# Kernel optimization log

Measured on AMD Instinct MI355X. Metric: run time of the kernel, lower is better.

The kernel has to match this reference:

```python
import jax, jax.numpy as jnp
import numpy as np
import math

EMBED = 256
NH = 8            # num_heads
HD = EMBED // NH  # head_dim = 32
LEVELS = 4
P = 4             # points per level
SUMP = LEVELS * P # 16
OFFSET_SCALE = 0.5
SPATIAL = ((80, 80), (40, 40), (20, 20), (10, 10))  # (H, W) per level
BS, LQ = 4, 4096
LV = sum(h * w for h, w in SPATIAL)  # 8500


def _offset_bias():
    # replicates _reset_parameters grid init for sampling_offsets.bias
    thetas = np.arange(NH, dtype=np.float32) * (2.0 * math.pi / NH)
    grid = np.stack([np.cos(thetas), np.sin(thetas)], -1)  # [NH,2]
    grid = grid / np.abs(grid).max(-1, keepdims=True)
    grid = np.tile(grid.reshape(NH, 1, 2), (1, SUMP, 1))   # [NH,SUMP,2]
    scaling = np.concatenate([np.arange(1, P + 1) for _ in range(LEVELS)]).reshape(1, SUMP, 1)
    grid = grid * scaling
    return jnp.asarray(grid.reshape(-1), dtype=jnp.float32)  # [NH*SUMP*2]


def setup_inputs() -> dict:
    key = jax.random.key(0)
    ks = jax.random.split(key, 8)
    xavier = lambda k, fi, fo: jax.random.uniform(k, (fi, fo), jnp.float32,
                                                  -math.sqrt(6.0 / (fi + fo)), math.sqrt(6.0 / (fi + fo)))
    return {
        "query": jax.random.normal(ks[0], (BS, LQ, EMBED), jnp.float32),
        "reference_points": jax.random.uniform(ks[1], (BS, LQ, 1, 4), jnp.float32),
        "value": jax.random.normal(ks[2], (BS, LV, EMBED), jnp.float32),
        # sampling_offsets: weight is zero-init in torch; use small random so offsets depend on query
        "W_off": jax.random.normal(ks[3], (EMBED, NH * SUMP * 2), jnp.float32) * 0.01,
        "b_off": _offset_bias(),
        "W_attn": jax.random.normal(ks[4], (EMBED, NH * SUMP), jnp.float32) * 0.01,
        "b_attn": jnp.zeros((NH * SUMP,), jnp.float32),
        "W_v": xavier(ks[5], EMBED, EMBED),
        "b_v": jnp.zeros((EMBED,), jnp.float32),
        "W_o": xavier(ks[6], EMBED, EMBED),
        "b_o": jnp.zeros((EMBED,), jnp.float32),
    }


def _bilinear_sample(v_l, loc, Hl, Wl):
    """grid_sample (bilinear, zero padding, align_corners=False) on one level.
    v_l: [bs, NH, Hl*Wl, HD]; loc: [bs, Lq, NH, P, 2] in [0,1] (x=width, y=height).
    Returns [bs, Lq, NH, P, HD]."""
    bs, lq, nh, p, _ = loc.shape
    x = loc[..., 0] * Wl - 0.5
    y = loc[..., 1] * Hl - 0.5
    x0 = jnp.floor(x)
    y0 = jnp.floor(y)
    lx, ly = x - x0, y - y0
    x0i = x0.astype(jnp.int32)
    y0i = y0.astype(jnp.int32)

    def corner(xi, yi, w):
        valid = ((xi >= 0) & (xi < Wl) & (yi >= 0) & (yi < Hl)).astype(v_l.dtype)
        idx = jnp.clip(yi, 0, Hl - 1) * Wl + jnp.clip(xi, 0, Wl - 1)  # [bs,Lq,NH,P]
        idx = jnp.transpose(idx, (0, 2, 1, 3)).reshape(bs, nh, lq * p)
        g = jnp.take_along_axis(v_l, idx[..., None], axis=2)          # [bs,NH,Lq*P,HD]
        g = g.reshape(bs, nh, lq, p, HD).transpose(0, 2, 1, 3, 4)     # [bs,Lq,NH,P,HD]
        return g * (w * valid)[..., None]

    return (corner(x0i, y0i, (1 - lx) * (1 - ly))
            + corner(x0i + 1, y0i, lx * (1 - ly))
            + corner(x0i, y0i + 1, (1 - lx) * ly)
            + corner(x0i + 1, y0i + 1, lx * ly))


def reference(query, reference_points, value, W_off, b_off, W_attn, b_attn, W_v, b_v, W_o, b_o):
    bs, lq = query.shape[:2]
    lv = value.shape[1]

    v = (value @ W_v + b_v).reshape(bs, lv, NH, HD)

    off = (query @ W_off + b_off).reshape(bs, lq, NH, SUMP, 2)
    attn = jax.nn.softmax((query @ W_attn + b_attn).reshape(bs, lq, NH, SUMP), axis=-1)

    # reference_points last dim == 4 path (box refs)
    nps = jnp.full((SUMP, 1), 1.0 / P, dtype=query.dtype)  # num_points_scale
    loc = (reference_points[:, :, None, :, :2]
           + off * nps * reference_points[:, :, None, :, 2:] * OFFSET_SCALE)  # [bs,Lq,NH,SUMP,2]

    out = jnp.zeros((bs, lq, NH, HD), dtype=query.dtype)
    v_start, p_start = 0, 0
    for (Hl, Wl) in SPATIAL:
        n = Hl * Wl
        v_l = jnp.transpose(v[:, v_start:v_start + n], (0, 2, 1, 3))  # [bs,NH,n,HD]
        loc_l = loc[:, :, :, p_start:p_start + P]
        w_l = attn[:, :, :, p_start:p_start + P]
        sampled = _bilinear_sample(v_l, loc_l, Hl, Wl)                # [bs,Lq,NH,P,HD]
        out = out + jnp.einsum('blhpd,blhp->blhd', sampled, w_l)
        v_start += n
        p_start += P

    return out.reshape(bs, lq, EMBED) @ W_o + b_o
```

## Files before the change

kernel.cpp:

```cpp
#include <hip/hip_runtime.h>

#define NH 8
#define HD 32
#define SUMP 16
#define LQ 4096
#define BS 4
#define LV 8500
#define NQ (BS * LQ)
#define MV (BS * LV)

typedef float f32x4 __attribute__((ext_vector_type(4)));
typedef _Float16 f16x8 __attribute__((ext_vector_type(8)));

__global__ __launch_bounds__(256) void prep_kernel(
    const float* __restrict__ Wv, const float* __restrict__ Woff,
    const float* __restrict__ Wattn, const float* __restrict__ Wo,
    const float* __restrict__ boff, const float* __restrict__ battn,
    _Float16* __restrict__ WtVf, _Float16* __restrict__ WtOAf,
    _Float16* __restrict__ WtOf, float* __restrict__ biasOA)
{
    int g = blockIdx.x * 256 + threadIdx.x;
    int gl; _Float16* dst; int which;
    if (g < 65536)       { gl = g;          dst = WtVf;  which = 0; }
    else if (g < 163840) { gl = g - 65536;  dst = WtOAf; which = 1; }
    else                 { gl = g - 163840; dst = WtOf;  which = 2; }
    int e = gl & 7, m16 = (gl >> 3) & 15, q = (gl >> 7) & 3, C = (gl >> 9) & 7, T = gl >> 12;
    int n = T * 16 + m16, k = C * 32 + q * 8 + e;
    float w;
    if (which == 0)      w = Wv[k * 256 + n];
    else if (which == 1) w = (n < 256) ? Woff[k * 256 + n] : Wattn[k * 128 + (n - 256)];
    else                 w = Wo[k * 256 + n];
    dst[gl] = (_Float16)w;
    if (blockIdx.x == 0) biasOA[threadIdx.x] = boff[threadIdx.x];
    if (blockIdx.x == 1 && threadIdx.x < 128) biasOA[256 + threadIdx.x] = battn[threadIdx.x];
}

__device__ __forceinline__ f16x8 cvt8(const float4& lo, const float4& hi) {
    f16x8 r;
    r[0] = (_Float16)lo.x; r[1] = (_Float16)lo.y; r[2] = (_Float16)lo.z; r[3] = (_Float16)lo.w;
    r[4] = (_Float16)hi.x; r[5] = (_Float16)hi.y; r[6] = (_Float16)hi.z; r[7] = (_Float16)hi.w;
    return r;
}

template <int NI, bool V_MODE, bool A_F16>
__device__ __forceinline__ void chunk_gemm(
    const float* __restrict__ A32, const _Float16* __restrict__ A16,
    const _Float16* __restrict__ Bf, const float* __restrict__ bias,
    void* __restrict__ Cv, int M, int N, int mchunk, int ntbase,
    _Float16* __restrict__ As )
{
    const int t = threadIdx.x;
    const int wave = t >> 6, lane = t & 63;
    const int quad = lane >> 4, l16 = lane & 15;

    {
        const int srow = t >> 2, schunk = t & 3;
        int gr = mchunk * 64 + srow;
        if (gr > M - 1) gr = M - 1;
        if (A_F16) {
            const _Float16* src = A16 + (size_t)gr * 256 + schunk * 64;
            f16x8 hb[8];
            #pragma unroll
            for (int j = 0; j < 8; ++j) hb[j] = *(const f16x8*)(src + j * 8);
            #pragma unroll
            for (int j = 0; j < 8; ++j) {
                int slot = (schunk * 8 + j) ^ (srow & 7);
                *(f16x8*)(As + srow * 256 + slot * 8) = hb[j];
            }
        } else {
            const float* src = A32 + (size_t)gr * 256 + schunk * 64;
            float4 buf[16];
            #pragma unroll
            for (int j = 0; j < 16; ++j) buf[j] = *(const float4*)(src + j * 4);
            #pragma unroll
            for (int j = 0; j < 8; ++j) {
                f16x8 h = cvt8(buf[2 * j], buf[2 * j + 1]);
                int slot = (schunk * 8 + j) ^ (srow & 7);
                *(f16x8*)(As + srow * 256 + slot * 8) = h;
            }
        }
    }
    __syncthreads();

    const int ntile0 = ntbase + wave * NI;
    const _Float16* bp[NI];
    #pragma unroll
    for (int ni = 0; ni < NI; ++ni)
        bp[ni] = Bf + (size_t)(ntile0 + ni) * 4096 + lane * 8;

    f16x8 bcur[NI], bnxt[NI];
    f32x4 acc[4][NI] = {};
    #pragma unroll
    for (int ni = 0; ni < NI; ++ni) bcur[ni] = *(const f16x8*)(bp[ni]);

    #pragma unroll
    for (int k = 0; k < 8; ++k) {
        if (k < 7) {
            #pragma unroll
            for (int ni = 0; ni < NI; ++ni) bnxt[ni] = *(const f16x8*)(bp[ni] + (k + 1) * 512);
        }
        f16x8 af[4];
        #pragma unroll
        for (int mi = 0; mi < 4; ++mi) {
            int row = mi * 16 + l16;
            int slot = (quad + k * 4) ^ (row & 7);
            af[mi] = *(const f16x8*)(As + row * 256 + slot * 8);
        }
        #pragma unroll
        for (int mi = 0; mi < 4; ++mi)
            #pragma unroll
            for (int ni = 0; ni < NI; ++ni)
                acc[mi][ni] = __builtin_amdgcn_mfma_f32_16x16x32_f16(af[mi], bcur[ni], acc[mi][ni], 0, 0, 0);
        if (k < 7) {
            #pragma unroll
            for (int ni = 0; ni < NI; ++ni) bcur[ni] = bnxt[ni];
        }
    }

    if (V_MODE) {
        #pragma unroll
        for (int mi = 0; mi < 4; ++mi) {
            int mq = mchunk * 64 + mi * 16 + quad * 4;
            size_t rb[4]; int vld[4];
            #pragma unroll
            for (int r = 0; r < 4; ++r) {
                int m = mq + r;
                vld[r] = (m < M);
                int mm = vld[r] ? m : 0;
                int b = mm / LV; int pos = mm - b * LV;
                rb[r] = ((size_t)b * NH * LV + pos) * 32;
            }
            #pragma unroll
            for (int ni = 0; ni < NI; ++ni) {
                int n = (ntile0 + ni) * 16 + l16;
                float bv = bias[n];
                int h = n >> 5, d = n & 31;
                size_t ho = (size_t)h * (LV * 32) + d;
                #pragma unroll
                for (int r = 0; r < 4; ++r)
                    if (vld[r]) ((_Float16*)Cv)[rb[r] + ho] = (_Float16)(acc[mi][ni][r] + bv);
            }
        }
    } else {
        #pragma unroll
        for (int ni = 0; ni < NI; ++ni) {
            int n = (ntile0 + ni) * 16 + l16;
            float bv = bias[n];
            #pragma unroll
            for (int mi = 0; mi < 4; ++mi) {
                int mq = mchunk * 64 + mi * 16 + quad * 4;
                #pragma unroll
                for (int r = 0; r < 4; ++r)
                    ((float*)Cv)[(size_t)(mq + r) * N + n] = acc[mi][ni][r] + bv;
            }
        }
    }
}

__global__ __launch_bounds__(256) void gemm_dual_kernel(
    const float* __restrict__ value, const _Float16* __restrict__ WtVf,
    const float* __restrict__ b_v, _Float16* __restrict__ v_f16,
    const float* __restrict__ query, const _Float16* __restrict__ WtOAf,
    const float* __restrict__ biasOA, float* __restrict__ oa)
{
    __shared__ __align__(16) _Float16 As[64 * 256];
    int bid = blockIdx.x;
    if (bid < 532) {
        chunk_gemm<4, true, false>(value, nullptr, WtVf, b_v, v_f16, MV, 256,
                                   bid, 0, As);
    } else {
        int g = bid - 532;
        chunk_gemm<3, false, false>(query, nullptr, WtOAf, biasOA, oa, NQ, 384,
                                    g >> 1, (g & 1) * 12, As);
    }
}

__global__ __launch_bounds__(256) void gemm_o_kernel(
    const _Float16* __restrict__ mid, const _Float16* __restrict__ WtOf,
    const float* __restrict__ b_o, float* __restrict__ out)
{
    __shared__ __align__(16) _Float16 As[64 * 256];
    chunk_gemm<4, false, true>(nullptr, mid, WtOf, b_o, out, NQ, 256,
                               blockIdx.x, 0, As);
}

__global__ void sample_kernel(
    const _Float16* __restrict__ v,
    const float* __restrict__ oa,
    const float* __restrict__ refp,
    _Float16* __restrict__ mid)
{
    const int blk = blockIdx.x;
    const int xcd = blk & 7, j = blk >> 3;
    const int bh = xcd * 4 + (j & 3);
    const int chunk = j >> 2;
    const int b = bh >> 3, h = bh & 7;
    const int rowG0 = b * LQ + chunk * 16;

    const int t = threadIdx.x;
    const int wave = t >> 6, lane = t & 63;

    __shared__ __align__(16) int2   s_pk[16 * 17];
    __shared__ __align__(16) float4 s_w4[16 * 17];
    __shared__ __align__(16) float  s_part[2 * 8 * 32];

    {
        int task = t >> 4, p = t & 15, l = p >> 2;
        int row = rowG0 + task;
        float4 r4 = *(const float4*)(refp + (size_t)row * 4);
        float2 o2 = *(const float2*)(oa + (size_t)row * 384 + (h * 16 + p) * 2);
        float raw = oa[(size_t)row * 384 + 256 + h * 16 + p];

        float mx = raw;
        #pragma unroll
        for (int d = 8; d >= 1; d >>= 1) mx = fmaxf(mx, __shfl_xor(mx, d, 16));
        float ex = __expf(raw - mx);
        float sm = ex;
        #pragma unroll
        for (int d = 8; d >= 1; d >>= 1) sm += __shfl_xor(sm, d, 16);
        float w = ex * __builtin_amdgcn_rcpf(sm);

        int Wl = 80 >> l;
        int vst = (l == 0) ? 0 : (l == 1) ? 6400 : (l == 2) ? 8000 : 8400;
        float x = (r4.x + o2.x * 0.125f * r4.z) * Wl - 0.5f;
        float y = (r4.y + o2.y * 0.125f * r4.w) * Wl - 0.5f;
        float x0f = floorf(x), y0f = floorf(y);
        float lx = x - x0f, ly = y - y0f;
        int x0 = (int)x0f, y0 = (int)y0f;
        int x1 = x0 + 1, y1 = y0 + 1;
        float mx0 = (x0 >= 0 && x0 < Wl) ? 1.f : 0.f;
        float mx1 = (x1 >= 0 && x1 < Wl) ? 1.f : 0.f;
        float my0 = (y0 >= 0 && y0 < Wl) ? 1.f : 0.f;
        float my1 = (y1 >= 0 && y1 < Wl) ? 1.f : 0.f;
        int cx0 = min(max(x0, 0), Wl - 1), cx1 = min(max(x1, 0), Wl - 1);
        int cy0 = min(max(y0, 0), Wl - 1), cy1 = min(max(y1, 0), Wl - 1);
        int2 r_pk;
        float4 r_w4;
        r_pk.x = (vst + cy0 * Wl + cx0) * 64;
        r_pk.y = ((cx1 - cx0) * 64) | (((cy1 - cy0) * Wl * 64) << 16);
        r_w4.x = w * (1.f - lx) * (1.f - ly) * mx0 * my0;
        r_w4.y = w * lx * (1.f - ly) * mx1 * my0;
        r_w4.z = w * (1.f - lx) * ly * mx0 * my1;
        r_w4.w = w * lx * ly * mx1 * my1;
        int s = task * 17 + p;
        s_pk[s] = r_pk; s_w4[s] = r_w4;
    }
    __syncthreads();

    {
        const int wg = wave >> 1, wp = wave & 1;
        const int pgl = lane >> 5, tk = (lane >> 2) & 7, dv2 = lane & 3;
        const int task = wg * 8 + tk;
        const int row = rowG0 + task;
        const char* vb = (const char*)v + ((size_t)(b * NH + h) * LV) * 64 + dv2 * 16;

        int2 pk[4]; float4 w4[4];
        #pragma unroll
        for (int jj = 0; jj < 4; ++jj) {
            int p = (wp * 2 + pgl) * 4 + jj;
            int s = task * 17 + p;
            pk[jj] = s_pk[s]; w4[jj] = s_w4[s];
        }
        f16x8 g0[4], g1[4], g2[4], g3[4];
        #pragma unroll
        for (int jj = 0; jj < 4; ++jj) {
            int dx = pk[jj].y & 0xffff, dy = pk[jj].y >> 16;
            const char* base = vb + pk[jj].x;
            g0[jj] = *(const f16x8*)(base);
            g1[jj] = *(const f16x8*)(base + dx);
            g2[jj] = *(const f16x8*)(base + dy);
            g3[jj] = *(const f16x8*)(base + dx + dy);
        }
        float acc8[8] = {};
        #pragma unroll
        for (int jj = 0; jj < 4; ++jj)
            #pragma unroll
            for (int c = 0; c < 8; ++c)
                acc8[c] += w4[jj].x * (float)g0[jj][c] + w4[jj].y * (float)g1[jj][c]
                         + w4[jj].z * (float)g2[jj][c] + w4[jj].w * (float)g3[jj][c];

        #pragma unroll
        for (int c = 0; c < 8; ++c) acc8[c] += __shfl_xor(acc8[c], 32, 64);
        if (wp == 1 && lane < 32) {
            #pragma unroll
            for (int c = 0; c < 8; ++c) s_part[wg * 256 + c * 32 + lane] = acc8[c];
        }
        __syncthreads();
        if (wp == 0 && lane < 32) {
            f16x8 m8;
            #pragma unroll
            for (int c = 0; c < 8; ++c)
                m8[c] = (_Float16)(acc8[c] + s_part[wg * 256 + c * 32 + lane]);
            *(f16x8*)(mid + (size_t)row * 256 + h * 32 + dv2 * 8) = m8;
        }
    }
}

extern "C" void kernel_launch(void* const* d_in, const int* in_sizes, int n_in,
                              void* d_out, int out_size, void* d_ws, size_t ws_size,
                              hipStream_t stream) {
    const float* query  = (const float*)d_in[0];
    const float* refp   = (const float*)d_in[1];
    const float* value  = (const float*)d_in[2];
    const float* W_off  = (const float*)d_in[3];
    const float* b_off  = (const float*)d_in[4];
    const float* W_attn = (const float*)d_in[5];
    const float* b_attn = (const float*)d_in[6];
    const float* W_v    = (const float*)d_in[7];
    const float* b_v    = (const float*)d_in[8];
    const float* W_o    = (const float*)d_in[9];
    const float* b_o    = (const float*)d_in[10];

    char* ws = (char*)d_ws;
    _Float16* v_f16  = (_Float16*)(ws + 0);
    float*    oa_f32 = (float*)(ws + 17408000);
    _Float16* mid    = (_Float16*)(ws + 42573824);
    _Float16* WtVf   = (_Float16*)(ws + 50962432);
    _Float16* WtOAf  = (_Float16*)(ws + 51093504);
    _Float16* WtOf   = (_Float16*)(ws + 51290112);
    float*    biasOA = (float*)(ws + 51421184);

    prep_kernel<<<896, 256, 0, stream>>>(W_v, W_off, W_attn, W_o, b_off, b_attn,
                                         WtVf, WtOAf, WtOf, biasOA);
    gemm_dual_kernel<<<1044, 256, 0, stream>>>(
        value, WtVf, b_v, v_f16, query, WtOAf, biasOA, oa_f32);
    sample_kernel<<<8192, 256, 0, stream>>>(v_f16, oa_f32, refp, mid);
    gemm_o_kernel<<<256, 256, 0, stream>>>(mid, WtOf, b_o, (float*)d_out);
}
```

Baseline: 169.0 us.

## Rewrite output GEMM with smaller tiles and more blocks; reorder sample point mapping

Replaces the shared chunk_gemm path for the output projection with a dedicated kernel that processes 32-row M chunks split into two N halves. The grid grows from 256 to 1024 blocks, and B fragments are prefetched from global one k-step ahead into registers. The goal is better CU occupancy for the small final GEMM, at the cost of loading each A tile twice and re-reading B more often. Separately, the sampling kernel changes how each lane's points map to levels, interleaving levels across lanes, which may alter gather locality.

```diff
diff --git a/kernel.cpp b/kernel.cpp
--- a/kernel.cpp
+++ b/kernel.cpp
@@ -179,9 +179,66 @@
     const _Float16* __restrict__ mid, const _Float16* __restrict__ WtOf,
     const float* __restrict__ b_o, float* __restrict__ out)
 {
-    __shared__ __align__(16) _Float16 As[64 * 256];
-    chunk_gemm<4, false, true>(nullptr, mid, WtOf, b_o, out, NQ, 256,
-                               blockIdx.x, 0, As);
+    __shared__ __align__(16) _Float16 As[32 * 256];
+    const int t = threadIdx.x;
+    const int wave = t >> 6, lane = t & 63;
+    const int quad = lane >> 4, l16 = lane & 15;
+    const int mchunk = blockIdx.x >> 1;
+    const int nc = blockIdx.x & 1;
+
+    {
+        const int srow = t >> 3, sc = t & 7;
+        const _Float16* src = mid + (size_t)(mchunk * 32 + srow) * 256 + sc * 32;
+        f16x8 hb[4];
+        #pragma unroll
+        for (int j = 0; j < 4; ++j) hb[j] = *(const f16x8*)(src + j * 8);
+        #pragma unroll
+        for (int j = 0; j < 4; ++j) {
+            int slot = (sc * 4 + j) ^ (srow & 7);
+            *(f16x8*)(As + srow * 256 + slot * 8) = hb[j];
+        }
+    }
+    __syncthreads();
+
+    const int wrow = wave >> 1, wcol = wave & 1;
+    const int ntile0 = nc * 8 + wcol * 4;
+    const _Float16* bp[4];
+    #pragma unroll
+    for (int ni = 0; ni < 4; ++ni)
+        bp[ni] = WtOf + (size_t)(ntile0 + ni) * 4096 + lane * 8;
+
+    f16x8 bcur[4], bnxt[4];
+    f32x4 acc[4] = {};
+    #pragma unroll
+    for (int ni = 0; ni < 4; ++ni) bcur[ni] = *(const f16x8*)(bp[ni]);
+
+    #pragma unroll
+    for (int k = 0; k < 8; ++k) {
+        if (k < 7) {
+            #pragma unroll
+            for (int ni = 0; ni < 4; ++ni) bnxt[ni] = *(const f16x8*)(bp[ni] + (k + 1) * 512);
+        }
+        const int row = wrow * 16 + l16;
+        const int slot = (quad + k * 4) ^ (row & 7);
+        f16x8 af = *(const f16x8*)(As + row * 256 + slot * 8);
+        #pragma unroll
+        for (int ni = 0; ni < 4; ++ni)
+            acc[ni] = __builtin_amdgcn_mfma_f32_16x16x32_f16(af, bcur[ni], acc[ni], 0, 0, 0);
+        if (k < 7) {
+            #pragma unroll
+            for (int ni = 0; ni < 4; ++ni) bcur[ni] = bnxt[ni];
+        }
+    }
+
+    #pragma unroll
+    for (int ni = 0; ni < 4; ++ni) {
+        int n = (ntile0 + ni) * 16 + l16;
+        float bv = b_o[n];
+        int mq = mchunk * 32 + wrow * 16 + quad * 4;
+        #pragma unroll
+        for (int r = 0; r < 4; ++r)
+            out[(size_t)(mq + r) * 256 + n] = acc[ni][r] + bv;
+    }
 }
 
 __global__ void sample_kernel(
@@ -257,7 +314,7 @@
         int2 pk[4]; float4 w4[4];
         #pragma unroll
         for (int jj = 0; jj < 4; ++jj) {
-            int p = (wp * 2 + pgl) * 4 + jj;
+            int p = jj * 4 + wp * 2 + pgl;
             int s = task * 17 + p;
             pk[jj] = s_pk[s]; w4[jj] = s_w4[s];
         }
@@ -325,5 +382,5 @@
     gemm_dual_kernel<<<1044, 256, 0, stream>>>(
         value, WtVf, b_v, v_f16, query, WtOAf, biasOA, oa_f32);
     sample_kernel<<<8192, 256, 0, stream>>>(v_f16, oa_f32, refp, mid);
-    gemm_o_kernel<<<256, 256, 0, stream>>>(mid, WtOf, b_o, (float*)d_out);
-}
+    gemm_o_kernel<<<1024, 256, 0, stream>>>(mid, WtOf, b_o, (float*)d_out);
+}
```

After: 170.8 us. About the same (+1.1%).
